# Optimization experiments

Hardware: AMD Instinct MI355X
Metric: run time of the kernel (lower is better)

Reference implementation:

```python
import jax, jax.numpy as jnp
import numpy as np


def setup_inputs() -> dict:
    key = jax.random.key(0)
    ks = jax.random.split(key, 7)
    B, H, W = 32, 28, 28
    C3, C4 = 1024, 2048
    C = C3 + C4            # 3072
    L1 = 9                 # num_landmarks + 1
    A, NC = 312, 200
    return {
        "l3": jax.random.normal(ks[0], (B, C3, H, W), jnp.float32),
        "l4": jax.random.normal(ks[1], (B, C4, H // 2, W // 2), jnp.float32),
        "conv_w": jax.random.normal(ks[2], (L1, C), jnp.float32) * 0.02,
        "modulation": jnp.ones((1, C, L1), jnp.float32),
        "attr_w": jax.random.normal(ks[3], (A, C), jnp.float32) * 0.02,
        "attr_b": jnp.zeros((A,), jnp.float32),
        "class_w": jax.random.normal(ks[4], (NC, A), jnp.float32) * 0.02,
    }


def reference(l3, l4, conv_w, modulation, attr_w, attr_b, class_w):
    b, c3, h, w = l3.shape
    # F.interpolate(l4, (h, w), mode='bilinear', align_corners=False)
    l4_up = jax.image.resize(l4, (b, l4.shape[1], h, w), method="bilinear")
    x = jnp.concatenate([l4_up, l3], axis=1)            # (b, 3072, h, w)

    # 1x1 conv: ab[b,l,h,w] = sum_c w[l,c] * x[b,c,h,w]
    ab = jnp.einsum("lc,bchw->blhw", conv_w, x)
    b_sq = jnp.sum(x * x, axis=1, keepdims=True)        # (b,1,h,w)
    a_sq = jnp.sum(conv_w, axis=1)[None, :, None, None]  # (1,L+1,1,1)  (matches torch: weight.sum(1), NOT squared)
    maps = jax.nn.softmax(-(b_sq - 2.0 * ab + a_sq), axis=1)  # Softmax2d = softmax over channels

    # (maps[:,None] * x[:,:,None]).mean((-1,-2))  ->  batched GEMM over spatial dim
    all_features = jnp.einsum("blhw,bchw->bcl", maps, x) / (h * w)  # (b, c, L+1)

    mod = all_features * modulation                     # dropout is identity at eval
    # permute(0,2,1)[:, :-1, :].mean(1) == mean over landmark dim excluding background
    mean_features = jnp.mean(mod[:, :, :-1], axis=2)    # (b, c)

    attr_scores = mean_features @ attr_w.T + attr_b      # (b, 312)
    class_scores = attr_scores @ class_w.T               # (b, 200)
    return attr_scores, class_scores, maps, all_features
```

## Files before the change

kernel.cpp:

```cpp
#include <hip/hip_runtime.h>
#include <math.h>

#define B_    32
#define C3_   1024
#define C4_   2048
#define C_    3072
#define P_    784
#define Q_    196
#define L_    9
#define NG_   25088
#define A_    312
#define NC_   200

#define ATTR_OFF  0
#define CLASS_OFF 9984
#define MAPS_OFF  16384
#define AF_OFF    242176

#define ASQ_OFF   0
#define MF_OFF    16
#define LOGITS_OFF 98320
#define Y_OFF     (LOGITS_OFF + 9 * NG_)
#define MP_OFF    (Y_OFF + 32 * 9 * Q_)

typedef __attribute__((ext_vector_type(8))) short bf16x8;
typedef __attribute__((ext_vector_type(4))) float f32x4;

__device__ __forceinline__ short f2bf(float f) {
    union { float f; unsigned u; } v; v.f = f;
    unsigned r = v.u + 0x7FFFu + ((v.u >> 16) & 1u);
    return (short)(r >> 16);
}

#define GLDS16(gp, lp) __builtin_amdgcn_global_load_lds(                    \
        (const __attribute__((address_space(1))) unsigned int*)(gp),        \
        (__attribute__((address_space(3))) unsigned int*)(lp), 16, 0, 0)

__global__ __launch_bounds__(256) void zK(const float* __restrict__ conv_w,
                                          float* __restrict__ zbase,
                                          float* __restrict__ asq) {
    int bx = blockIdx.x, t = threadIdx.x;
    if (bx < 9) {
        __shared__ float red[256];
        const float4* w = (const float4*)(conv_w + (size_t)bx * C_);
        float s = 0.f;
#pragma unroll
        for (int i = 0; i < 3; ++i) {
            float4 v = w[t + i * 256];
            s += v.x + v.y + v.z + v.w;
        }
        red[t] = s; __syncthreads();
        for (int o = 128; o > 0; o >>= 1) {
            if (t < o) red[t] += red[t + o];
            __syncthreads();
        }
        if (t == 0) asq[bx] = red[0];
        return;
    }
    int i = (bx - 9) * 256 + t;
    if (i < 70560)
        ((float4*)zbase)[i] = make_float4(0.f, 0.f, 0.f, 0.f);
}

__global__ __launch_bounds__(256, 5) void kA(
        const float* __restrict__ l3, const float* __restrict__ l4,
        const float* __restrict__ conv_w,
        float* __restrict__ logits, float* __restrict__ Y) {
    __shared__ float X[2][16 * 256];
    int bid = blockIdx.x;
    int t = threadIdx.x;
    int wave = t >> 6, lane = t & 63;

    bool isl3 = (bid < 1568);
    int slab = 0, g0 = 0, b = 0, grp = 0, cbase_w;
    const float* gbase;
    size_t rowpitch;
    if (isl3) {
        slab = bid / 98;
        g0 = (bid % 98) * 256;
        int gidx = g0 + lane * 4;
        int bb = gidx / 784, px = gidx % 784;
        gbase = l3 + ((size_t)bb * C3_ + slab * 64) * P_ + px;
        rowpitch = P_;
        cbase_w = C4_ + slab * 64;
    } else {
        int idx = bid - 1568;
        b = idx >> 5; grp = idx & 31;
        int q = lane * 4;
        if (q > 192) q = 192;
        gbase = l4 + ((size_t)b * C4_ + grp * 64) * Q_ + q;
        rowpitch = Q_;
        cbase_w = grp * 64;
    }

#pragma unroll
    for (int r = 0; r < 4; ++r) {
        int row = wave * 4 + r;
        GLDS16(gbase + (size_t)row * rowpitch, &X[0][row * 256]);
    }

    float acc[9];
#pragma unroll
    for (int l = 0; l < 9; ++l) acc[l] = 0.f;

#pragma unroll
    for (int j = 0; j < 4; ++j) {
        const int cur = j & 1;
        if (j < 3) {
#pragma unroll
            for (int r = 0; r < 4; ++r) {
                int row = wave * 4 + r;
                int ch = (j + 1) * 16 + row;
                GLDS16(gbase + (size_t)ch * rowpitch, &X[cur ^ 1][row * 256]);
            }
            asm volatile("s_waitcnt vmcnt(4)" ::: "memory");
        } else {
            asm volatile("s_waitcnt vmcnt(0)" ::: "memory");
        }
        __builtin_amdgcn_s_barrier();

        if (isl3 || t < 196) {
#pragma unroll
            for (int c = 0; c < 16; ++c) {
                float x = X[cur][c * 256 + t];
#pragma unroll
                for (int l = 0; l < 9; ++l)
                    acc[l] = fmaf(conv_w[(size_t)l * C_ + cbase_w + j * 16 + c],
                                  x, acc[l]);
            }
        }
        __builtin_amdgcn_s_barrier();
    }

    if (isl3) {
#pragma unroll
        for (int l = 0; l < 9; ++l)
            atomicAdd(&logits[(size_t)l * NG_ + g0 + t], 2.f * acc[l]);
    } else if (t < 196) {
#pragma unroll
        for (int l = 0; l < 9; ++l)
            atomicAdd(&Y[((size_t)b * 9 + l) * Q_ + t], acc[l]);
    }
}

__global__ __launch_bounds__(256) void kC(const float* __restrict__ logits,
                                          const float* __restrict__ Y,
                                          const float* __restrict__ asq,
                                          float* __restrict__ out_maps) {
    int g = blockIdx.x * 256 + threadIdx.x;
    int b = g / P_, p = g % P_;
    int yy = p / 28, xx = p % 28;
    float sy = 0.5f * yy - 0.25f, sx = 0.5f * xx - 0.25f;
    float fyf = floorf(sy), fxf = floorf(sx);
    float fy = sy - fyf, fx = sx - fxf;
    int ya = max(0, (int)fyf), yb = min(13, (int)fyf + 1);
    int xa = max(0, (int)fxf), xb = min(13, (int)fxf + 1);
    float w00 = (1.f - fy) * (1.f - fx), w01 = (1.f - fy) * fx;
    float w10 = fy * (1.f - fx),         w11 = fy * fx;
    float v[9];
#pragma unroll
    for (int l = 0; l < 9; ++l) {
        const float* Yl = Y + ((size_t)b * 9 + l) * Q_;
        float ab4 = w00 * Yl[ya * 14 + xa] + w01 * Yl[ya * 14 + xb]
                  + w10 * Yl[yb * 14 + xa] + w11 * Yl[yb * 14 + xb];
        v[l] = logits[(size_t)l * NG_ + g] + 2.f * ab4 - asq[l];
    }
    float m = v[0];
#pragma unroll
    for (int l = 1; l < 9; ++l) m = fmaxf(m, v[l]);
    float sum = 0.f;
#pragma unroll
    for (int l = 0; l < 9; ++l) { v[l] = expf(v[l] - m); sum += v[l]; }
    float inv = 1.f / sum;
#pragma unroll
    for (int l = 0; l < 9; ++l)
        out_maps[(size_t)b * (L_ * P_) + l * P_ + p] = v[l] * inv;
}

__device__ __forceinline__ int adj_taps(int q, int* ys, float* wy) {
    if (q == 0)  { ys[0] = 0;  wy[0] = 1.00f; ys[1] = 1;  wy[1] = 0.75f;
                   ys[2] = 2;  wy[2] = 0.25f; return 3; }
    if (q == 13) { ys[0] = 25; wy[0] = 0.25f; ys[1] = 26; wy[1] = 0.75f;
                   ys[2] = 27; wy[2] = 1.00f; return 3; }
    ys[0] = 2 * q - 1; wy[0] = 0.25f;
    ys[1] = 2 * q;     wy[1] = 0.75f;
    ys[2] = 2 * q + 1; wy[2] = 0.75f;
    ys[3] = 2 * q + 2; wy[3] = 0.25f;
    return 4;
}

__global__ __launch_bounds__(256) void kD(const float* __restrict__ maps,
                                          float* __restrict__ Mp) {
    int tid = blockIdx.x * 256 + threadIdx.x;
    if (tid >= 32 * 9 * Q_) return;
    int b = tid / (9 * Q_);
    int r = tid % (9 * Q_);
    int l = r / Q_, q = r % Q_;
    int qy = q / 14, qx = q % 14;
    int ys[4], xs[4]; float wy[4], wx[4];
    int ny = adj_taps(qy, ys, wy);
    int nx = adj_taps(qx, xs, wx);
    const float* mrow = maps + (size_t)b * (L_ * P_) + l * P_;
    float s = 0.f;
    for (int i = 0; i < ny; ++i) {
        float rs = 0.f;
        for (int j = 0; j < nx; ++j)
            rs = fmaf(wx[j], mrow[ys[i] * 28 + xs[j]], rs);
        s = fmaf(wy[i], rs, s);
    }
    Mp[(size_t)b * (9 * Q_) + r] = s;
}

__global__ __launch_bounds__(256, 3) void kE(
        const float* __restrict__ l3, const float* __restrict__ l4,
        const float* __restrict__ maps, const float* __restrict__ Mp,
        const float* __restrict__ mod,
        float* __restrict__ out_af, float* __restrict__ mf) {
    __shared__ float sAf[576];
    int bid = blockIdx.x;
    int t = threadIdx.x;
    int wave = t >> 6, lane = t & 63;
    int row16 = lane & 15, quad = lane >> 4;

    bool isl4 = (bid < 1024);
    int b, c0, nchunk, cglob0, pitch;
    const float* xsrc; const float* bsrc;
    if (isl4) {
        b = bid >> 5; c0 = (bid & 31) * 64; nchunk = 1;
        xsrc = l4 + ((size_t)b * C4_ + c0) * Q_;
        bsrc = Mp + (size_t)b * (9 * Q_);
        pitch = Q_;
        cglob0 = c0;
    } else {
        int idx = bid - 1024;
        b = idx >> 4; c0 = (idx & 15) * 64; nchunk = 4;
        xsrc = l3 + ((size_t)b * C3_ + c0) * P_;
        bsrc = maps + (size_t)b * (L_ * P_);
        pitch = P_;
        cglob0 = C4_ + c0;
    }
    const float* arow = xsrc + (size_t)(wave * 16 + row16) * pitch;
    const float* brow = bsrc + (size_t)row16 * pitch;

    f32x4 acc = {0.f, 0.f, 0.f, 0.f};
    for (int h = 0; h < nchunk; ++h) {
        int koff = h * 196;
        float4 a[13];
#pragma unroll
        for (int s = 0; s < 6; ++s) {
            int k0 = koff + s * 32 + quad * 8;
            a[2 * s]     = *(const float4*)(arow + k0);
            a[2 * s + 1] = *(const float4*)(arow + k0 + 4);
        }
        a[12] = make_float4(0.f, 0.f, 0.f, 0.f);
        if (quad == 0) a[12] = *(const float4*)(arow + koff + 192);

        bf16x8 bfr[7];
#pragma unroll
        for (int s = 0; s < 7; ++s) {
            int k0 = s * 32 + quad * 8;
            bf16x8 bv = {0, 0, 0, 0, 0, 0, 0, 0};
            if (row16 < 9) {
                const float* bp = brow + koff + k0;
                if (s < 6) {
                    float4 b0 = *(const float4*)(bp);
                    float4 b1 = *(const float4*)(bp + 4);
                    bv[0] = f2bf(b0.x); bv[1] = f2bf(b0.y);
                    bv[2] = f2bf(b0.z); bv[3] = f2bf(b0.w);
                    bv[4] = f2bf(b1.x); bv[5] = f2bf(b1.y);
                    bv[6] = f2bf(b1.z); bv[7] = f2bf(b1.w);
                } else if (quad == 0) {
                    float4 b0 = *(const float4*)(bp);
                    bv[0] = f2bf(b0.x); bv[1] = f2bf(b0.y);
                    bv[2] = f2bf(b0.z); bv[3] = f2bf(b0.w);
                }
            }
            bfr[s] = bv;
        }

#pragma unroll
        for (int s = 0; s < 7; ++s) {
            bf16x8 av = {0, 0, 0, 0, 0, 0, 0, 0};
            if (s < 6) {
                float4 a0 = a[2 * s], a1 = a[2 * s + 1];
                av[0] = f2bf(a0.x); av[1] = f2bf(a0.y);
                av[2] = f2bf(a0.z); av[3] = f2bf(a0.w);
                av[4] = f2bf(a1.x); av[5] = f2bf(a1.y);
                av[6] = f2bf(a1.z); av[7] = f2bf(a1.w);
            } else if (quad == 0) {
                float4 a0 = a[12];
                av[0] = f2bf(a0.x); av[1] = f2bf(a0.y);
                av[2] = f2bf(a0.z); av[3] = f2bf(a0.w);
            }
            acc = __builtin_amdgcn_mfma_f32_16x16x32_bf16(av, bfr[s], acc,
                                                          0, 0, 0);
        }
    }

    int l = row16;
    int lc = wave * 16 + quad * 4;
    float afv[4];
#pragma unroll
    for (int r = 0; r < 4; ++r) afv[r] = acc[r] * (1.f / 784.f);
    if (l < 9) {
#pragma unroll
        for (int r = 0; r < 4; ++r) sAf[(lc + r) * 9 + l] = afv[r];
    }
    int cg = cglob0 + lc;
    float term[4];
#pragma unroll
    for (int r = 0; r < 4; ++r)
        term[r] = (l < 8) ? afv[r] * mod[(size_t)(cg + r) * 9 + l] : 0.f;
#pragma unroll
    for (int s = 1; s < 16; s <<= 1)
#pragma unroll
        for (int r = 0; r < 4; ++r) term[r] += __shfl_xor(term[r], s);
    if (row16 == 0) {
#pragma unroll
        for (int r = 0; r < 4; ++r)
            mf[(size_t)b * C_ + cg + r] = term[r] * 0.125f;
    }
    __syncthreads();
    size_t obase = ((size_t)b * C_ + cglob0) * 9;
    if (t < 144)
        ((float4*)(out_af + obase))[t] = ((const float4*)sAf)[t];
}

__global__ __launch_bounds__(256) void kF(
        const float* __restrict__ mf, const float* __restrict__ attr_w,
        const float* __restrict__ attr_b, float* __restrict__ out_attr) {
    __shared__ float sw[C_];
    int a = blockIdx.x, t = threadIdx.x;
    const float4* wr = (const float4*)(attr_w + (size_t)a * C_);
#pragma unroll
    for (int i = 0; i < 3; ++i)
        ((float4*)sw)[t + i * 256] = wr[t + i * 256];
    __syncthreads();

    int b = t >> 3, j = t & 7;
    const float* mrow = mf + (size_t)b * C_;
    float acc = 0.f;
#pragma unroll 8
    for (int m = 0; m < 96; ++m) {
        int k = j * 4 + m * 32;
        float4 mv = *(const float4*)(mrow + k);
        float4 wv = *(const float4*)(sw + k);
        acc += mv.x * wv.x + mv.y * wv.y + mv.z * wv.z + mv.w * wv.w;
    }
    acc += __shfl_xor(acc, 1);
    acc += __shfl_xor(acc, 2);
    acc += __shfl_xor(acc, 4);
    if (j == 0) out_attr[(size_t)b * A_ + a] = acc + attr_b[a];
}

__global__ __launch_bounds__(256) void kG(
        const float* __restrict__ attr, const float* __restrict__ class_w,
        float* __restrict__ out_class) {
    int idx = blockIdx.x * 4 + (threadIdx.x >> 6);
    int lane = threadIdx.x & 63;
    int b = idx / NC_, n = idx % NC_;
    float acc = 0.f;
    for (int a = lane; a < A_; a += 64)
        acc += attr[b * A_ + a] * class_w[n * A_ + a];
    acc += __shfl_xor(acc, 1);  acc += __shfl_xor(acc, 2);
    acc += __shfl_xor(acc, 4);  acc += __shfl_xor(acc, 8);
    acc += __shfl_xor(acc, 16); acc += __shfl_xor(acc, 32);
    if (lane == 0) out_class[idx] = acc;
}

extern "C" void kernel_launch(void* const* d_in, const int* in_sizes, int n_in,
                              void* d_out, int out_size, void* d_ws, size_t ws_size,
                              hipStream_t stream) {
    (void)in_sizes; (void)n_in; (void)out_size; (void)ws_size;
    const float* l3         = (const float*)d_in[0];
    const float* l4         = (const float*)d_in[1];
    const float* conv_w     = (const float*)d_in[2];
    const float* modulation = (const float*)d_in[3];
    const float* attr_w     = (const float*)d_in[4];
    const float* attr_b     = (const float*)d_in[5];
    const float* class_w    = (const float*)d_in[6];
    float* out = (float*)d_out;
    float* ws  = (float*)d_ws;
    float* asq    = ws + ASQ_OFF;
    float* mf     = ws + MF_OFF;
    float* logits = ws + LOGITS_OFF;
    float* Y      = ws + Y_OFF;
    float* Mp     = ws + MP_OFF;

    zK<<<285, 256, 0, stream>>>(conv_w, logits , asq);
    kA<<<2592, 256, 0, stream>>>(l3, l4, conv_w, logits, Y);
    kC<<<98, 256, 0, stream>>>(logits, Y, asq, out + MAPS_OFF);
    kD<<<221, 256, 0, stream>>>(out + MAPS_OFF, Mp);
    kE<<<1536, 256, 0, stream>>>(l3, l4, out + MAPS_OFF, Mp, modulation,
                                 out + AF_OFF, mf);
    kF<<<A_, 256, 0, stream>>>(mf, attr_w, attr_b, out + ATTR_OFF);
    kG<<<(B_ * NC_) / 4, 256, 0, stream>>>(out + ATTR_OFF, class_w,
                                           out + CLASS_OFF);
}
```

Baseline: 268.7 us.

## Retile l3 logits blocks to full images with contiguous 8-channel staging

The l3 part of kA now gives each block one batch image and a 64-channel slab. It stages 8 channels of all 784 pixels at a time as contiguous chunks into double-buffered LDS, and each thread accumulates 4 pixels × 9 landmarks. The l3 grid shrinks from 1568 blocks to 512, which reduces per-block overhead and the weight reloads per pixel. The cost is more registers and LDS per block (launch bounds drop to 3 blocks per unit), fewer blocks for parallelism, and a partial last wave for the 16-pixel tail.

New measurement: 268.2 us. About the same (-0.2%).

```diff
diff --git a/kernel.cpp b/kernel.cpp
--- a/kernel.cpp
+++ b/kernel.cpp
@@ -62,41 +62,97 @@
         ((float4*)zbase)[i] = make_float4(0.f, 0.f, 0.f, 0.f);
 }
 
-__global__ __launch_bounds__(256, 5) void kA(
+__global__ __launch_bounds__(256, 3) void kA(
         const float* __restrict__ l3, const float* __restrict__ l4,
         const float* __restrict__ conv_w,
         float* __restrict__ logits, float* __restrict__ Y) {
-    __shared__ float X[2][16 * 256];
+    __shared__ float X[2][8 * 784];
     int bid = blockIdx.x;
     int t = threadIdx.x;
     int wave = t >> 6, lane = t & 63;
 
-    bool isl3 = (bid < 1568);
-    int slab = 0, g0 = 0, b = 0, grp = 0, cbase_w;
-    const float* gbase;
-    size_t rowpitch;
-    if (isl3) {
-        slab = bid / 98;
-        g0 = (bid % 98) * 256;
-        int gidx = g0 + lane * 4;
-        int bb = gidx / 784, px = gidx % 784;
-        gbase = l3 + ((size_t)bb * C3_ + slab * 64) * P_ + px;
-        rowpitch = P_;
-        cbase_w = C4_ + slab * 64;
-    } else {
-        int idx = bid - 1568;
-        b = idx >> 5; grp = idx & 31;
-        int q = lane * 4;
-        if (q > 192) q = 192;
-        gbase = l4 + ((size_t)b * C4_ + grp * 64) * Q_ + q;
-        rowpitch = Q_;
-        cbase_w = grp * 64;
-    }
+    if (bid < 512) {
+        int b = bid >> 4, slab = bid & 15;
+        const float* region = l3 + ((size_t)b * C3_ + slab * 64) * P_;
+        int cbase_w = C4_ + slab * 64;
+
+        auto stage = [&](int cc, int buf) {
+            const float* src = region + (size_t)cc * 6272;
+#pragma unroll
+            for (int i = 0; i < 6; ++i) {
+                int j = i * 4 + wave;
+                GLDS16(src + j * 256 + lane * 4, &X[buf][j * 256]);
+            }
+            if (wave == 3 && lane < 32)
+                GLDS16(src + 6144 + lane * 4, &X[buf][6144]);
+        };
+
+        stage(0, 0);
+
+        float acc[9][4];
+#pragma unroll
+        for (int l = 0; l < 9; ++l)
+#pragma unroll
+            for (int pi = 0; pi < 4; ++pi) acc[l][pi] = 0.f;
+
+        for (int c = 0; c < 8; ++c) {
+            int cur = c & 1;
+            if (c < 7) {
+                stage(c + 1, cur ^ 1);
+                if (wave == 3)
+                    asm volatile("s_waitcnt vmcnt(7)" ::: "memory");
+                else
+                    asm volatile("s_waitcnt vmcnt(6)" ::: "memory");
+            } else {
+                asm volatile("s_waitcnt vmcnt(0)" ::: "memory");
+            }
+            __builtin_amdgcn_s_barrier();
+
+#pragma unroll
+            for (int r = 0; r < 8; ++r) {
+                float x0 = X[cur][r * 784 + t];
+                float x1 = X[cur][r * 784 + t + 256];
+                float x2 = X[cur][r * 784 + t + 512];
+                float x3 = (t < 16) ? X[cur][r * 784 + 768 + t] : 0.f;
+#pragma unroll
+                for (int l = 0; l < 9; ++l) {
+                    float wv = conv_w[(size_t)l * C_ + cbase_w + c * 8 + r];
+                    acc[l][0] = fmaf(wv, x0, acc[l][0]);
+                    acc[l][1] = fmaf(wv, x1, acc[l][1]);
+                    acc[l][2] = fmaf(wv, x2, acc[l][2]);
+                    acc[l][3] = fmaf(wv, x3, acc[l][3]);
+                }
+            }
+            __builtin_amdgcn_s_barrier();
+        }
+
+        size_t gb = (size_t)b * P_;
+#pragma unroll
+        for (int l = 0; l < 9; ++l) {
+            atomicAdd(&logits[(size_t)l * NG_ + gb + t],       2.f * acc[l][0]);
+            atomicAdd(&logits[(size_t)l * NG_ + gb + t + 256], 2.f * acc[l][1]);
+            atomicAdd(&logits[(size_t)l * NG_ + gb + t + 512], 2.f * acc[l][2]);
+        }
+        if (t < 16) {
+#pragma unroll
+            for (int l = 0; l < 9; ++l)
+                atomicAdd(&logits[(size_t)l * NG_ + gb + 768 + t],
+                          2.f * acc[l][3]);
+        }
+        return;
+    }
+
+    int idx = bid - 512;
+    int b = idx >> 5, grp = idx & 31;
+    int q = lane * 4;
+    if (q > 192) q = 192;
+    const float* gbase = l4 + ((size_t)b * C4_ + grp * 64) * Q_ + q;
+    int cbase_w = grp * 64;
 
 #pragma unroll
     for (int r = 0; r < 4; ++r) {
         int row = wave * 4 + r;
-        GLDS16(gbase + (size_t)row * rowpitch, &X[0][row * 256]);
+        GLDS16(gbase + (size_t)row * Q_, &X[0][row * 256]);
     }
 
     float acc[9];
@@ -111,7 +167,7 @@
             for (int r = 0; r < 4; ++r) {
                 int row = wave * 4 + r;
                 int ch = (j + 1) * 16 + row;
-                GLDS16(gbase + (size_t)ch * rowpitch, &X[cur ^ 1][row * 256]);
+                GLDS16(gbase + (size_t)ch * Q_, &X[cur ^ 1][row * 256]);
             }
             asm volatile("s_waitcnt vmcnt(4)" ::: "memory");
         } else {
@@ -119,7 +175,7 @@
         }
         __builtin_amdgcn_s_barrier();
 
-        if (isl3 || t < 196) {
+        if (t < 196) {
 #pragma unroll
             for (int c = 0; c < 16; ++c) {
                 float x = X[cur][c * 256 + t];
@@ -132,11 +188,7 @@
         __builtin_amdgcn_s_barrier();
     }
 
-    if (isl3) {
-#pragma unroll
-        for (int l = 0; l < 9; ++l)
-            atomicAdd(&logits[(size_t)l * NG_ + g0 + t], 2.f * acc[l]);
-    } else if (t < 196) {
+    if (t < 196) {
 #pragma unroll
         for (int l = 0; l < 9; ++l)
             atomicAdd(&Y[((size_t)b * 9 + l) * Q_ + t], acc[l]);
@@ -388,7 +440,7 @@
     float* Mp     = ws + MP_OFF;
 
     zK<<<285, 256, 0, stream>>>(conv_w, logits , asq);
-    kA<<<2592, 256, 0, stream>>>(l3, l4, conv_w, logits, Y);
+    kA<<<1536, 256, 0, stream>>>(l3, l4, conv_w, logits, Y);
     kC<<<98, 256, 0, stream>>>(logits, Y, asq, out + MAPS_OFF);
     kD<<<221, 256, 0, stream>>>(out + MAPS_OFF, Mp);
     kE<<<1536, 256, 0, stream>>>(l3, l4, out + MAPS_OFF, Mp, modulation,
```
